# Optimization experiments

Hardware: AMD Instinct MI355X
Metric: run time of the kernel (lower is better)

The kernel has to match this reference:

```python
import jax, jax.numpy as jnp
import numpy as np
from jax import lax

VOCAB, EMBED, HID, MID = 32000, 200, 10, 5
BSZ, SEQ = 256, 512
LN_EPS = 1e-5


def setup_inputs() -> dict:
    key = jax.random.key(0)
    ks = jax.random.split(key, 10)
    s = 0.1
    return {
        "src_tokens": jax.random.randint(ks[0], (BSZ, SEQ), 0, VOCAB, dtype=jnp.int64)
        if jax.config.jax_enable_x64 else jax.random.randint(ks[0], (BSZ, SEQ), 0, VOCAB, dtype=jnp.int32),
        "h0": jax.random.normal(ks[1], (1, BSZ, HID), jnp.float32),
        "c0": jax.random.normal(ks[2], (1, BSZ, HID), jnp.float32),
        "embed_W": jax.random.normal(ks[3], (VOCAB, EMBED), jnp.float32),
        "W_ih": jax.random.normal(ks[4], (4 * HID, EMBED), jnp.float32) * s,
        "W_hh": jax.random.normal(ks[5], (4 * HID, HID), jnp.float32) * s,
        "b_ih": jax.random.normal(ks[6], (4 * HID,), jnp.float32) * s,
        "b_hh": jax.random.normal(ks[7], (4 * HID,), jnp.float32) * s,
        "W1": jax.random.normal(ks[8], (MID, HID), jnp.float32) * s,
        "b1": jnp.zeros((MID,), jnp.float32),
        "ln_g": jnp.ones((MID,), jnp.float32),
        "ln_b": jnp.zeros((MID,), jnp.float32),
        "W2": jax.random.normal(ks[9], (1, MID), jnp.float32) * s,
        "b2": jnp.zeros((1,), jnp.float32),
    }


def reference(src_tokens, h0, c0, embed_W, W_ih, W_hh, b_ih, b_hh,
              W1, b1, ln_g, ln_b, W2, b2):
    # Embedding lookup -> [B, S, E] -> time-major [S, B, E]
    x = embed_W[src_tokens].astype(jnp.float32)
    x = jnp.transpose(x, (1, 0, 2))
    # Precompute input contribution to all 4 gates (i,f,g,o order, as torch)
    gates_x = jnp.einsum('sbe,ge->sbg', x, W_ih) + b_ih + b_hh  # [S, B, 4H]

    def step(carry, gx):
        h, c = carry
        gates = gx + h @ W_hh.T
        i, f, g, o = jnp.split(gates, 4, axis=-1)
        i = jax.nn.sigmoid(i)
        f = jax.nn.sigmoid(f)
        g = jnp.tanh(g)
        o = jax.nn.sigmoid(o)
        c = f * c + i * g
        h = o * jnp.tanh(c)
        return (h, c), None

    (hn, _), _ = lax.scan(step, (h0[0], c0[0]), gates_x)  # hn: [B, H]

    z = hn @ W1.T + b1  # [B, 5]
    mu = jnp.mean(z, axis=-1, keepdims=True)
    var = jnp.mean(jnp.square(z - mu), axis=-1, keepdims=True)
    z = (z - mu) * lax.rsqrt(var + LN_EPS) * ln_g + ln_b
    out = jax.nn.sigmoid(z @ W2.T + b2)  # [B, 1]
    return out[:, 0]  # squeeze -> [B]
```

## Files before the change

kernel.cpp:

```cpp
#include <hip/hip_runtime.h>
#include <math.h>

#define VOCAB 32000
#define EMBED 200
#define HID   10
#define GATES 40
#define BSZ   256
#define SEQ   512
#define PF    8

#define RPB   64
#define KCH   8
#define WROW  48

__device__ __forceinline__ float rcp_fast(float x) { return __builtin_amdgcn_rcpf(x); }
__device__ __forceinline__ float exp2_fast(float x) { return __builtin_amdgcn_exp2f(x); }
__device__ __forceinline__ float readlane_f(float v, int l) {
    return __int_as_float(__builtin_amdgcn_readlane(__float_as_int(v), l));
}
template <int Q>
__device__ __forceinline__ float quad_bcast(float v) {
    return __int_as_float(__builtin_amdgcn_mov_dpp(
        __float_as_int(v), Q * 0x55, 0xF, 0xF, true));
}

__global__ __launch_bounds__(256) void proj_kernel(
    const float* __restrict__ embed, const float* __restrict__ Wih,
    const float* __restrict__ bih,   const float* __restrict__ bhh,
    float* __restrict__ proj)
{
    __shared__ float wT[EMBED * WROW];
    __shared__ float eT[RPB * (KCH + 1)];

    const int tid = threadIdx.x;
    const int tr  = tid & 63;
    const int tg  = tid >> 6;
    const int v0  = blockIdx.x * RPB;

    for (int idx = tid; idx < GATES * EMBED; idx += 256) {
        int g = idx / EMBED, k = idx - g * EMBED;
        wT[k * WROW + (g / 10) * 12 + (g % 10)] = Wih[idx];
    }

    float acc[10];
    #pragma unroll
    for (int i = 0; i < 10; ++i) acc[i] = 0.f;

    for (int k0 = 0; k0 < EMBED; k0 += KCH) {
        __syncthreads();
        {
            int idx0 = tid;
            int r0 = idx0 >> 3, c0 = idx0 & 7;
            eT[r0 * (KCH + 1) + c0] = embed[(size_t)(v0 + r0) * EMBED + k0 + c0];
            int idx1 = tid + 256;
            int r1 = idx1 >> 3, c1 = idx1 & 7;
            eT[r1 * (KCH + 1) + c1] = embed[(size_t)(v0 + r1) * EMBED + k0 + c1];
        }
        __syncthreads();

        #pragma unroll
        for (int kk = 0; kk < KCH; ++kk) {
            float e = eT[tr * (KCH + 1) + kk];
            const float* wr = &wT[(k0 + kk) * WROW + tg * 12];
            float4 wa = *(const float4*)(wr);
            float4 wb = *(const float4*)(wr + 4);
            float2 wc = *(const float2*)(wr + 8);
            acc[0] = fmaf(e, wa.x, acc[0]);
            acc[1] = fmaf(e, wa.y, acc[1]);
            acc[2] = fmaf(e, wa.z, acc[2]);
            acc[3] = fmaf(e, wa.w, acc[3]);
            acc[4] = fmaf(e, wb.x, acc[4]);
            acc[5] = fmaf(e, wb.y, acc[5]);
            acc[6] = fmaf(e, wb.z, acc[6]);
            acc[7] = fmaf(e, wb.w, acc[7]);
            acc[8] = fmaf(e, wc.x, acc[8]);
            acc[9] = fmaf(e, wc.y, acc[9]);
        }
    }

    const int gbase = tg * 10;
    float* op = &proj[(size_t)(v0 + tr) * GATES + gbase];
    #pragma unroll
    for (int i = 0; i < 5; ++i) {
        float2 o;
        o.x = acc[2 * i]     + bih[gbase + 2 * i]     + bhh[gbase + 2 * i];
        o.y = acc[2 * i + 1] + bih[gbase + 2 * i + 1] + bhh[gbase + 2 * i + 1];
        *(float2*)(op + 2 * i) = o;
    }
}

__global__ __launch_bounds__(64) void lstm_rec(
    const int*   __restrict__ tok,  const float* __restrict__ proj,
    const float* __restrict__ h0,   const float* __restrict__ c0,
    const float* __restrict__ Whh,
    const float* __restrict__ W1,   const float* __restrict__ b1,
    const float* __restrict__ lng,  const float* __restrict__ lnb,
    const float* __restrict__ W2,   const float* __restrict__ b2,
    float* __restrict__ out)
{
    __shared__ int tok_s[SEQ + 2 * PF];

    const int b    = blockIdx.x;
    const int lane = threadIdx.x;
    const int j0   = min(lane >> 2, HID - 1);
    const int k4   = lane & 3;
    const int gate = k4 * HID + j0;

    #pragma unroll
    for (int k = 0; k < SEQ / 64; ++k)
        tok_s[k * 64 + lane] = tok[b * SEQ + k * 64 + lane];
    if (lane < 2 * PF) tok_s[SEQ + lane] = 0;
    __syncthreads();

    float w[HID];
    #pragma unroll
    for (int j = 0; j < HID; ++j) w[j] = Whh[gate * HID + j];

    float hs[HID];
    #pragma unroll
    for (int u = 0; u < HID; ++u) hs[u] = h0[b * HID + u];
    float c_own = c0[b * HID + j0];

    const float am  = (k4 == 2) ? 2.f : 1.f;
    const float amc = 1.f - am;
    const float amn = -1.442695041f * am;

    int   tk_cur[PF], tk_nxt[PF];
    float gx_cur[PF], gx_nxt[PF];
    #pragma unroll
    for (int k = 0; k < PF; ++k) tk_cur[k] = tok_s[k];
    #pragma unroll
    for (int k = 0; k < PF; ++k) gx_cur[k] = proj[tk_cur[k] * GATES + gate];
    #pragma unroll
    for (int k = 0; k < PF; ++k) tk_nxt[k] = tok_s[PF + k];

    for (int s0 = 0; s0 < SEQ; s0 += PF) {
        #pragma unroll
        for (int k = 0; k < PF; ++k)
            gx_nxt[k] = proj[tk_nxt[k] * GATES + gate];
        #pragma unroll
        for (int k = 0; k < PF; ++k)
            tk_cur[k] = tok_s[s0 + 2 * PF + k];

        #pragma unroll
        for (int k = 0; k < PF; ++k) {
            float a0 = gx_cur[k], a1 = 0.f;
            a0 = fmaf(hs[0], w[0], a0); a1 = fmaf(hs[1], w[1], a1);
            a0 = fmaf(hs[2], w[2], a0); a1 = fmaf(hs[3], w[3], a1);
            a0 = fmaf(hs[4], w[4], a0); a1 = fmaf(hs[5], w[5], a1);
            a0 = fmaf(hs[6], w[6], a0); a1 = fmaf(hs[7], w[7], a1);
            a0 = fmaf(hs[8], w[8], a0); a1 = fmaf(hs[9], w[9], a1);
            float acc = a0 + a1;

            float t   = exp2_fast(amn * acc);
            float sg  = rcp_fast(1.f + t);
            float val = fmaf(am, sg, amc);

            float iv = quad_bcast<0>(val);
            float fv = quad_bcast<1>(val);
            float gv = quad_bcast<2>(val);
            float ov = quad_bcast<3>(val);

            c_own = fmaf(fv, c_own, iv * gv);
            float t2 = exp2_fast(c_own * -2.885390082f);
            float th = fmaf(2.f, rcp_fast(1.f + t2), -1.f);
            float h_own = ov * th;

            hs[0] = readlane_f(h_own, 0);  hs[1] = readlane_f(h_own, 4);
            hs[2] = readlane_f(h_own, 8);  hs[3] = readlane_f(h_own, 12);
            hs[4] = readlane_f(h_own, 16); hs[5] = readlane_f(h_own, 20);
            hs[6] = readlane_f(h_own, 24); hs[7] = readlane_f(h_own, 28);
            hs[8] = readlane_f(h_own, 32); hs[9] = readlane_f(h_own, 36);
        }

        #pragma unroll
        for (int k = 0; k < PF; ++k) {
            gx_cur[k] = gx_nxt[k];
            int tmp = tk_cur[k];
            tk_nxt[k] = tmp;
        }
    }

    if (lane == 0) {
        float z[5];
        float mu = 0.f;
        #pragma unroll
        for (int m = 0; m < 5; ++m) {
            float a = b1[m];
            #pragma unroll
            for (int j = 0; j < HID; ++j) a = fmaf(hs[j], W1[m * HID + j], a);
            z[m] = a; mu += a;
        }
        mu *= 0.2f;
        float var = 0.f;
        #pragma unroll
        for (int m = 0; m < 5; ++m) { float d = z[m] - mu; var = fmaf(d, d, var); }
        var *= 0.2f;
        float rs = rsqrtf(var + 1e-5f);
        float acc = b2[0];
        #pragma unroll
        for (int m = 0; m < 5; ++m) {
            float zn = fmaf((z[m] - mu) * rs, lng[m], lnb[m]);
            acc = fmaf(zn, W2[m], acc);
        }
        out[b] = 1.f / (1.f + __expf(-acc));
    }
}

extern "C" void kernel_launch(void* const* d_in, const int* in_sizes, int n_in,
                              void* d_out, int out_size, void* d_ws, size_t ws_size,
                              hipStream_t stream) {
    const int*   tok   = (const int*)  d_in[0];
    const float* h0    = (const float*)d_in[1];
    const float* c0    = (const float*)d_in[2];
    const float* embed = (const float*)d_in[3];
    const float* Wih   = (const float*)d_in[4];
    const float* Whh   = (const float*)d_in[5];
    const float* bih   = (const float*)d_in[6];
    const float* bhh   = (const float*)d_in[7];
    const float* W1    = (const float*)d_in[8];
    const float* b1    = (const float*)d_in[9];
    const float* lng   = (const float*)d_in[10];
    const float* lnb   = (const float*)d_in[11];
    const float* W2    = (const float*)d_in[12];
    const float* b2    = (const float*)d_in[13];
    float* out  = (float*)d_out;
    float* proj = (float*)d_ws;

    hipLaunchKernelGGL(proj_kernel, dim3(VOCAB / RPB), dim3(256), 0, stream,
                       embed, Wih, bih, bhh, proj);
    hipLaunchKernelGGL(lstm_rec, dim3(BSZ), dim3(64), 0, stream,
                       tok, proj, h0, c0, Whh, W1, b1, lng, lnb, W2, b2, out);
}
```

Before: 95.86 us.

## Fold activation scale into projection table and W_hh, split recurrence FMA chains

The projection kernel now multiplies each gate's precomputed input contribution by the exp2 scaling constant (sigmoid or tanh). The recurrent weights are pre-scaled the same way, which removes one multiply from the serial per-step critical path. The dot product over the hidden state is split into four accumulator chains to shorten the dependency depth. The projection kernel also stages a full 64-row embedding tile in shared memory with float4 global loads and one barrier, replacing the per-8-column chunk loop with its repeated syncs, at the cost of much more LDS per block.

Measured after the change: 99.02 us. 3.3% more time.

```diff
diff --git a/kernel.cpp b/kernel.cpp
--- a/kernel.cpp
+++ b/kernel.cpp
@@ -9,9 +9,9 @@
 #define SEQ   512
 #define PF    8
 
-#define RPB   64
-#define KCH   8
-#define WROW  48
+#define RPB    64
+#define EPITCH 202
+#define WROW   48
 
 __device__ __forceinline__ float rcp_fast(float x) { return __builtin_amdgcn_rcpf(x); }
 __device__ __forceinline__ float exp2_fast(float x) { return __builtin_amdgcn_exp2f(x); }
@@ -24,72 +24,80 @@
         __float_as_int(v), Q * 0x55, 0xF, 0xF, true));
 }
 
-__global__ __launch_bounds__(256) void proj_kernel(
+#define SC_SIG (-1.442695041f)
+#define SC_TNH (-2.885390082f)
+
+__global__ __launch_bounds__(256, 1) void proj_kernel(
     const float* __restrict__ embed, const float* __restrict__ Wih,
     const float* __restrict__ bih,   const float* __restrict__ bhh,
     float* __restrict__ proj)
 {
+    __shared__ float eT[RPB * EPITCH];
     __shared__ float wT[EMBED * WROW];
-    __shared__ float eT[RPB * (KCH + 1)];
 
     const int tid = threadIdx.x;
-    const int tr  = tid & 63;
-    const int tg  = tid >> 6;
     const int v0  = blockIdx.x * RPB;
 
     for (int idx = tid; idx < GATES * EMBED; idx += 256) {
         int g = idx / EMBED, k = idx - g * EMBED;
         wT[k * WROW + (g / 10) * 12 + (g % 10)] = Wih[idx];
     }
+    {
+        const float4* src = (const float4*)(embed + (size_t)v0 * EMBED);
+        for (int f = tid; f < RPB * 50; f += 256) {
+            float4 x = src[f];
+            int r = f / 50, c = f - r * 50;
+            float* dst = &eT[r * EPITCH + c * 4];
+            dst[0] = x.x; dst[1] = x.y; dst[2] = x.z; dst[3] = x.w;
+        }
+    }
+    __syncthreads();
+
+    const int tr = tid & 63;
+    const int tg = tid >> 6;
 
     float acc[10];
     #pragma unroll
     for (int i = 0; i < 10; ++i) acc[i] = 0.f;
 
-    for (int k0 = 0; k0 < EMBED; k0 += KCH) {
-        __syncthreads();
-        {
-            int idx0 = tid;
-            int r0 = idx0 >> 3, c0 = idx0 & 7;
-            eT[r0 * (KCH + 1) + c0] = embed[(size_t)(v0 + r0) * EMBED + k0 + c0];
-            int idx1 = tid + 256;
-            int r1 = idx1 >> 3, c1 = idx1 & 7;
-            eT[r1 * (KCH + 1) + c1] = embed[(size_t)(v0 + r1) * EMBED + k0 + c1];
-        }
-        __syncthreads();
-
-        #pragma unroll
-        for (int kk = 0; kk < KCH; ++kk) {
-            float e = eT[tr * (KCH + 1) + kk];
+    for (int k0 = 0; k0 < EMBED; k0 += 8) {
+        float2 e01 = *(const float2*)&eT[tr * EPITCH + k0];
+        float2 e23 = *(const float2*)&eT[tr * EPITCH + k0 + 2];
+        float2 e45 = *(const float2*)&eT[tr * EPITCH + k0 + 4];
+        float2 e67 = *(const float2*)&eT[tr * EPITCH + k0 + 6];
+        float e[8] = {e01.x, e01.y, e23.x, e23.y, e45.x, e45.y, e67.x, e67.y};
+        #pragma unroll
+        for (int kk = 0; kk < 8; ++kk) {
             const float* wr = &wT[(k0 + kk) * WROW + tg * 12];
             float4 wa = *(const float4*)(wr);
             float4 wb = *(const float4*)(wr + 4);
             float2 wc = *(const float2*)(wr + 8);
-            acc[0] = fmaf(e, wa.x, acc[0]);
-            acc[1] = fmaf(e, wa.y, acc[1]);
-            acc[2] = fmaf(e, wa.z, acc[2]);
-            acc[3] = fmaf(e, wa.w, acc[3]);
-            acc[4] = fmaf(e, wb.x, acc[4]);
-            acc[5] = fmaf(e, wb.y, acc[5]);
-            acc[6] = fmaf(e, wb.z, acc[6]);
-            acc[7] = fmaf(e, wb.w, acc[7]);
-            acc[8] = fmaf(e, wc.x, acc[8]);
-            acc[9] = fmaf(e, wc.y, acc[9]);
-        }
-    }
-
+            acc[0] = fmaf(e[kk], wa.x, acc[0]);
+            acc[1] = fmaf(e[kk], wa.y, acc[1]);
+            acc[2] = fmaf(e[kk], wa.z, acc[2]);
+            acc[3] = fmaf(e[kk], wa.w, acc[3]);
+            acc[4] = fmaf(e[kk], wb.x, acc[4]);
+            acc[5] = fmaf(e[kk], wb.y, acc[5]);
+            acc[6] = fmaf(e[kk], wb.z, acc[6]);
+            acc[7] = fmaf(e[kk], wb.w, acc[7]);
+            acc[8] = fmaf(e[kk], wc.x, acc[8]);
+            acc[9] = fmaf(e[kk], wc.y, acc[9]);
+        }
+    }
+
+    const float sc = (tg == 2) ? SC_TNH : SC_SIG;
     const int gbase = tg * 10;
     float* op = &proj[(size_t)(v0 + tr) * GATES + gbase];
     #pragma unroll
     for (int i = 0; i < 5; ++i) {
         float2 o;
-        o.x = acc[2 * i]     + bih[gbase + 2 * i]     + bhh[gbase + 2 * i];
-        o.y = acc[2 * i + 1] + bih[gbase + 2 * i + 1] + bhh[gbase + 2 * i + 1];
+        o.x = (acc[2*i]   + bih[gbase + 2*i]   + bhh[gbase + 2*i])   * sc;
+        o.y = (acc[2*i+1] + bih[gbase + 2*i+1] + bhh[gbase + 2*i+1]) * sc;
         *(float2*)(op + 2 * i) = o;
     }
 }
 
-__global__ __launch_bounds__(64) void lstm_rec(
+__global__ __launch_bounds__(64, 1) void lstm_rec(
     const int*   __restrict__ tok,  const float* __restrict__ proj,
     const float* __restrict__ h0,   const float* __restrict__ c0,
     const float* __restrict__ Whh,
@@ -112,19 +120,19 @@
     if (lane < 2 * PF) tok_s[SEQ + lane] = 0;
     __syncthreads();
 
+    const float am  = (k4 == 2) ? 2.f : 1.f;
+    const float amc = 1.f - am;
+    const float amn = (k4 == 2) ? SC_TNH : SC_SIG;
+
     float w[HID];
     #pragma unroll
-    for (int j = 0; j < HID; ++j) w[j] = Whh[gate * HID + j];
+    for (int j = 0; j < HID; ++j) w[j] = amn * Whh[gate * HID + j];
 
     float hs[HID];
     #pragma unroll
     for (int u = 0; u < HID; ++u) hs[u] = h0[b * HID + u];
     float c_own = c0[b * HID + j0];
 
-    const float am  = (k4 == 2) ? 2.f : 1.f;
-    const float amc = 1.f - am;
-    const float amn = -1.442695041f * am;
-
     int   tk_cur[PF], tk_nxt[PF];
     float gx_cur[PF], gx_nxt[PF];
     #pragma unroll
@@ -144,15 +152,15 @@
 
         #pragma unroll
         for (int k = 0; k < PF; ++k) {
-            float a0 = gx_cur[k], a1 = 0.f;
+            float a0 = gx_cur[k], a1 = 0.f, a2 = 0.f, a3 = 0.f;
             a0 = fmaf(hs[0], w[0], a0); a1 = fmaf(hs[1], w[1], a1);
-            a0 = fmaf(hs[2], w[2], a0); a1 = fmaf(hs[3], w[3], a1);
+            a2 = fmaf(hs[2], w[2], a2); a3 = fmaf(hs[3], w[3], a3);
             a0 = fmaf(hs[4], w[4], a0); a1 = fmaf(hs[5], w[5], a1);
-            a0 = fmaf(hs[6], w[6], a0); a1 = fmaf(hs[7], w[7], a1);
+            a2 = fmaf(hs[6], w[6], a2); a3 = fmaf(hs[7], w[7], a3);
             a0 = fmaf(hs[8], w[8], a0); a1 = fmaf(hs[9], w[9], a1);
-            float acc = a0 + a1;
-
-            float t   = exp2_fast(amn * acc);
+            float dt = (a0 + a2) + (a1 + a3);
+
+            float t   = exp2_fast(dt);
             float sg  = rcp_fast(1.f + t);
             float val = fmaf(am, sg, amc);
 
@@ -162,7 +170,7 @@
             float ov = quad_bcast<3>(val);
 
             c_own = fmaf(fv, c_own, iv * gv);
-            float t2 = exp2_fast(c_own * -2.885390082f);
+            float t2 = exp2_fast(c_own * SC_TNH);
             float th = fmaf(2.f, rcp_fast(1.f + t2), -1.f);
             float h_own = ov * th;
 
@@ -176,8 +184,7 @@
         #pragma unroll
         for (int k = 0; k < PF; ++k) {
             gx_cur[k] = gx_nxt[k];
-            int tmp = tk_cur[k];
-            tk_nxt[k] = tmp;
+            tk_nxt[k] = tk_cur[k];
         }
     }
 
```
